# Performance work log

Measured on AMD Instinct MI355X. Metric: run time of the kernel, lower is better.

## Reference

```python
import math
import jax, jax.numpy as jnp
import numpy as np

B, P, DC, NB, H = 32768, 16, 128, 32, 256
BOUND = 10.0
MIN_W = 1e-5
MIN_H = 1e-5
MIN_D = 1e-5
L2PI = 0.5 * math.log(2.0 * math.pi)


def setup_inputs() -> dict:
    key = jax.random.key(0)
    k0, k1, k2, k3 = jax.random.split(key, 4)
    x = jax.random.normal(k0, (B, P, 4), jnp.float32)
    c = jax.random.normal(k1, (B, P, DC), jnp.float32)
    W1 = jax.random.normal(k2, (DC, H), jnp.float32) / np.float32(np.sqrt(DC))
    b1 = jnp.zeros((H,), jnp.float32)
    # small init so spline params start near-identity-ish (typical subnet init)
    W2 = jax.random.normal(k3, (H, 3 * NB + 1), jnp.float32) * np.float32(0.1 / np.sqrt(H))
    b2 = jnp.zeros((3 * NB + 1,), jnp.float32)
    return {"x": x, "c": c, "W1": W1, "b1": b1, "W2": W2, "b2": b2}


def _pad_left_zero(a):
    # pad a zero at the start of the last axis
    pads = [(0, 0)] * (a.ndim - 1) + [(1, 0)]
    return jnp.pad(a, pads)


def _rqs_forward(x, theta):
    """Unconstrained rational-quadratic spline, forward direction.
    x: (B, P); theta: (B, P, 3*NB+1). Returns (z, log|det|), each (B, P)."""
    left, right, bottom, top = -BOUND, BOUND, -BOUND, BOUND
    inside = (x >= left) & (x <= right)

    uw = theta[..., :NB]
    uh = theta[..., NB:2 * NB]
    ud = theta[..., 2 * NB:]  # (B, P, NB+1)

    widths = MIN_W + (1.0 - MIN_W * NB) * jax.nn.softmax(uw, axis=-1)
    cumw = (right - left) * _pad_left_zero(jnp.cumsum(widths, axis=-1)) + left
    cumw = cumw.at[..., 0].set(left).at[..., -1].set(right)
    widths = cumw[..., 1:] - cumw[..., :-1]

    heights = MIN_H + (1.0 - MIN_H * NB) * jax.nn.softmax(uh, axis=-1)
    cumh = (top - bottom) * _pad_left_zero(jnp.cumsum(heights, axis=-1)) + bottom
    cumh = cumh.at[..., 0].set(bottom).at[..., -1].set(top)
    heights = cumh[..., 1:] - cumh[..., :-1]

    derivs = MIN_D + jax.nn.softplus(ud)  # (B, P, NB+1)

    xs = jnp.clip(x, left, right)
    # bin search: index of the bin containing xs
    bin_idx = jnp.clip(jnp.sum(xs[..., None] >= cumw, axis=-1) - 1, 0, NB - 1)
    idx = bin_idx[..., None]

    def g(a):
        return jnp.take_along_axis(a, idx, axis=-1)[..., 0]

    in_cw = g(cumw[..., :-1])
    in_w = g(widths)
    in_ch = g(cumh[..., :-1])
    in_h = g(heights)
    d0 = g(derivs[..., :-1])
    d1 = g(derivs[..., 1:])
    delta = in_h / in_w

    th = (xs - in_cw) / in_w
    th_om = th * (1.0 - th)
    numerator = in_h * (delta * th * th + d0 * th_om)
    denominator = delta + (d0 + d1 - 2.0 * delta) * th_om
    out = in_ch + numerator / denominator

    deriv_num = delta * delta * (d1 * th * th + 2.0 * delta * th_om + d0 * (1.0 - th) ** 2)
    logabsdet = jnp.log(deriv_num) - 2.0 * jnp.log(denominator)

    z = jnp.where(inside, out, x)
    jac = jnp.where(inside, logabsdet, jnp.zeros_like(x))
    return z, jac


def reference(x, c, W1, b1, W2, b2):
    # subnet MLP: c (B, P, DC) -> theta (B, P, 3*NB+1)
    h = jax.nn.relu(jnp.einsum("bpd,dh->bph", c, W1) + b1)
    theta = jnp.einsum("bph,hk->bpk", h, W2) + b2
    z, jac = _rqs_forward(x[..., -1], theta)
    prob = -L2PI - 0.5 * z * z + jac  # (B, P)
    return prob.sum(axis=1)  # (B,)
```

## Files before the change

### kernel.cpp

```cpp
#include <hip/hip_runtime.h>
#include <math.h>

#define NBLK 256
#define NTHR 512
#define PAIRS 8

typedef float  f32x4  __attribute__((ext_vector_type(4)));
typedef float  f32x16 __attribute__((ext_vector_type(16)));
typedef __bf16 bf16x8 __attribute__((ext_vector_type(8)));
typedef unsigned int u32x4 __attribute__((ext_vector_type(4)));

#define W1S 272
#define W2S 528
#define LDS_W1T 0
#define LDS_W2T 69632
#define LDS_B1  137216
#define LDS_B2  138240
#define LDS_TOTAL 138752

#define L2PIF 0.9189385332046727f
#define AW (1.0f - 32.0f*1e-5f)

__device__ __forceinline__ void mfma_v(f32x16& acc, bf16x8 a, bf16x8 b) {
    asm("s_nop 1\n\tv_mfma_f32_32x32x16_bf16 %0, %1, %2, %0"
        : "+v"(acc) : "v"(a), "v"(b));
}
__device__ __forceinline__ void mfma_a(f32x16& acc, bf16x8 a, bf16x8 b) {
    asm("s_nop 1\n\tv_mfma_f32_32x32x16_bf16 %0, %1, %2, %0"
        : "+a"(acc) : "v"(a), "v"(b));
}
__device__ __forceinline__ void mfma_a_init(f32x16& acc, bf16x8 a, bf16x8 b) {
    asm("s_nop 1\n\tv_mfma_f32_32x32x16_bf16 %0, %1, %2, 0"
        : "=a"(acc) : "v"(a), "v"(b));
}
__device__ __forceinline__ void mfma_fence_va(f32x16& v0, f32x16& a1) {
    asm("s_nop 7\n\ts_nop 7\n\ts_nop 7" : "+v"(v0), "+a"(a1));
}
__device__ __forceinline__ void mfma_fence4(f32x16& a0, f32x16& a1,
                                            f32x16& a2, f32x16& a3) {
    asm("s_nop 7\n\ts_nop 7\n\ts_nop 7"
        : "+a"(a0), "+a"(a1), "+a"(a2), "+a"(a3));
}

__device__ __forceinline__ void pl32swap(unsigned &a, unsigned &b) {
#if __has_builtin(__builtin_amdgcn_permlane32_swap)
    auto r = __builtin_amdgcn_permlane32_swap(a, b, false, false);
    a = (unsigned)r[0]; b = (unsigned)r[1];
#else
    asm("v_permlane32_swap_b32 %0, %1" : "+v"(a), "+v"(b));
#endif
}
__device__ __forceinline__ float sum32(float x) {
    unsigned a = __float_as_uint(x), b = a;
    pl32swap(a, b);
    return __uint_as_float(a) + __uint_as_float(b);
}
__device__ __forceinline__ float part32(float x) {
    unsigned u = __float_as_uint(x), a = u, b = u;
    pl32swap(a, b);
    return __uint_as_float(a ^ b ^ u);
}

__device__ __forceinline__ float rcpf(float x) {
#if __has_builtin(__builtin_amdgcn_rcpf)
    return __builtin_amdgcn_rcpf(x);
#else
    return 1.f / x;
#endif
}

template<int CTRL>
__device__ __forceinline__ float dppf(float v) {
    return __int_as_float(__builtin_amdgcn_update_dpp(
        0, __float_as_int(v), CTRL, 0xF, 0xF, false));
}
__device__ __forceinline__ float rorsum16(float x) {
    x += dppf<0x121>(x);
    x += dppf<0x122>(x);
    x += dppf<0x124>(x);
    x += dppf<0x128>(x);
    return x;
}
__device__ __forceinline__ float softplus_s(float u) {
    return fmaxf(u, 0.f) + __logf(1.f + __expf(-fabsf(u)));
}
__device__ __forceinline__ unsigned packbf(float a, float b) {
    unsigned short ua = __builtin_bit_cast(unsigned short, (__bf16)a);
    unsigned short ub = __builtin_bit_cast(unsigned short, (__bf16)b);
    return (unsigned)ua | ((unsigned)ub << 16);
}
__device__ __forceinline__ bf16x8 cvt8(f32x4 a, f32x4 b) {
    bf16x8 r;
    r[0]=(__bf16)a[0]; r[1]=(__bf16)a[1]; r[2]=(__bf16)a[2]; r[3]=(__bf16)a[3];
    r[4]=(__bf16)b[0]; r[5]=(__bf16)b[1]; r[6]=(__bf16)b[2]; r[7]=(__bf16)b[3];
    return r;
}

__device__ __forceinline__ void cum_softmax(const f32x16& tv, const char* bias,
                                            int h, float hf, float hoff,
                                            float* a, float* pw0)
{
    float bs0, bs1, bs2, bs3;
    #pragma unroll
    for (int m = 0; m < 4; ++m) {
        f32x4 bv = *(const f32x4*)(bias + m*32);
        float e0 = __expf(tv[4*m+0] + bv[0]);
        float e1 = __expf(tv[4*m+1] + bv[1]);
        float e2 = __expf(tv[4*m+2] + bv[2]);
        float e3 = __expf(tv[4*m+3] + bv[3]);
        a[4*m+0] = e0; a[4*m+1] = e1; a[4*m+2] = e2; a[4*m+3] = e3;
        float s = (e0 + e1) + (e2 + e3);
        if (m == 0) bs0 = s; else if (m == 1) bs1 = s;
        else if (m == 2) bs2 = s; else bs3 = s;
    }
    float t0 = sum32(bs0), t1 = sum32(bs1), t2 = sum32(bs2), t3 = sum32(bs3);
    float T1 = t0, T2 = T1 + t1, T3 = T2 + t2, S = T3 + t3;
    float sc = (20.f * AW) * rcpf(S);
    float st0 = hf * (t0 - bs0);
    float st1 = T1 + hf * (t1 - bs1);
    float st2 = T2 + hf * (t2 - bs2);
    float st3 = T3 + hf * (t3 - bs3);
    pw0[0] = fmaf(sc, st0, hoff);
    pw0[1] = fmaf(sc, st1, hoff + 1.6e-3f);
    pw0[2] = fmaf(sc, st2, hoff + 3.2e-3f);
    pw0[3] = fmaf(sc, st3, hoff + 4.8e-3f);
    #pragma unroll
    for (int m = 0; m < 4; ++m) {
        float run = (m == 0) ? st0 : (m == 1) ? st1 : (m == 2) ? st2 : st3;
        #pragma unroll
        for (int e = 0; e < 4; ++e) {
            run += a[4*m+e];
            a[4*m+e] = hoff + fmaf(sc, run, 2.0e-4f*(float)(8*m + e + 1));
        }
    }
    if (h) a[15] = 10.f;
}

__global__ __launch_bounds__(NTHR)
__attribute__((amdgpu_waves_per_eu(2)))
void flow_kernel(const float* __restrict__ x, const float* __restrict__ c,
                 const float* __restrict__ W1, const float* __restrict__ b1,
                 const float* __restrict__ W2, const float* __restrict__ b2,
                 float* __restrict__ out)
{
    extern __shared__ char smem[];
    const int tid  = threadIdx.x;
    const int wave = tid >> 6;
    const int lane = tid & 63;
    const int p    = lane & 31;
    const int h    = lane >> 5;
    const float hf   = (float)h;
    const float hoff = h ? (8.0e-4f - 10.f) : -10.f;

    {
        const f32x4* W1v = (const f32x4*)W1;
        for (int it = 0; it < 16; ++it) {
            int f4i = tid + it*NTHR;
            int d  = f4i >> 6;
            int j0 = (f4i & 63) << 2;
            f32x4 v = W1v[f4i];
            #pragma unroll
            for (int e = 0; e < 4; ++e) {
                int j = j0 + e;
                *(__bf16*)(smem + LDS_W1T + j*W1S + d*2) = (__bf16)v[e];
            }
        }
        const f32x4* W2v = (const f32x4*)W2;
        for (int f4i = tid; f4i < 6208; f4i += NTHR) {
            f32x4 v = W2v[f4i];
            #pragma unroll
            for (int e = 0; e < 4; ++e) {
                int lin = f4i*4 + e;
                int j = lin / 97;
                int q = lin - j*97;
                *(__bf16*)(smem + LDS_W2T + q*W2S + j*2) = (__bf16)v[e];
            }
        }
        for (int i = tid; i < 31*256; i += NTHR) {
            int q = 97 + (i >> 8);
            int j = i & 255;
            *(__bf16*)(smem + LDS_W2T + q*W2S + j*2) = (__bf16)0.f;
        }
        float* b1s = (float*)(smem + LDS_B1);
        float* b2s = (float*)(smem + LDS_B2);
        if (tid < 256) b1s[tid] = b1[tid];
        if (tid < 128) b2s[tid] = (tid < 97) ? b2[tid] : 0.f;
    }
    __syncthreads();

    const char* w1b = smem + LDS_W1T + p*W1S + h*16;
    const char* w2b = smem + LDS_W2T + p*W2S + h*16;
    const char* bb1 = smem + LDS_B1 + h*16;
    const char* bb2 = smem + LDS_B2 + h*16;

    const int base = blockIdx.x*128 + wave*16;

    bf16x8 cfrag[8];
    {
        const float* crow = c + (size_t)(base*16 + p)*128 + h*8;
        #pragma unroll
        for (int s = 0; s < 8; ++s)
            cfrag[s] = cvt8(*(const f32x4*)(crow + s*16),
                            *(const f32x4*)(crow + s*16 + 4));
    }
    float xr = x[(size_t)(base*16 + p)*4 + 3];

    for (int itn = 0; itn < PAIRS; ++itn) {
        const int t0 = base + itn*2;
        const int tn = (itn + 1 < PAIRS) ? (t0 + 2) : t0;
        const float* crow_n = c + (size_t)(tn*16 + p)*128 + h*8;

        f32x16 g2[4];
        f32x4  pf[6];
        bf16x8 cfrag_n[8];

        __builtin_amdgcn_s_setprio(1);

        #pragma unroll
        for (int jt = 0; jt < 8; ++jt) {
            pf[(jt % 3)*2]     = *(const f32x4*)(crow_n + jt*16);
            pf[(jt % 3)*2 + 1] = *(const f32x4*)(crow_n + jt*16 + 4);

            f32x16 g1a;
            #pragma unroll
            for (int m = 0; m < 4; ++m) {
                f32x4 bv = *(const f32x4*)(bb1 + jt*128 + m*32);
                g1a[4*m+0] = bv[0]; g1a[4*m+1] = bv[1];
                g1a[4*m+2] = bv[2]; g1a[4*m+3] = bv[3];
            }
            f32x16 g1b;
            #pragma unroll
            for (int s = 0; s < 4; ++s) {
                bf16x8 wa0 = *(const bf16x8*)(w1b + jt*32*W1S + s*32);
                bf16x8 wa1 = *(const bf16x8*)(w1b + jt*32*W1S + (s+4)*32);
                mfma_v(g1a, wa0, cfrag[s]);
                if (s == 0) mfma_a_init(g1b, wa1, cfrag[4]);
                else        mfma_a(g1b, wa1, cfrag[s+4]);
            }
            mfma_fence_va(g1a, g1b);
            unsigned P[8];
            #pragma unroll
            for (int m = 0; m < 4; ++m) {
                float v0 = fmaxf(g1a[4*m+0] + g1b[4*m+0], 0.f);
                float v1 = fmaxf(g1a[4*m+1] + g1b[4*m+1], 0.f);
                float v2 = fmaxf(g1a[4*m+2] + g1b[4*m+2], 0.f);
                float v3 = fmaxf(g1a[4*m+3] + g1b[4*m+3], 0.f);
                P[2*m]   = packbf(v0, v1);
                P[2*m+1] = packbf(v2, v3);
            }
            #pragma unroll
            for (int cc = 0; cc < 2; ++cc) {
                unsigned fa = P[4*cc+0], fb = P[4*cc+2];
                pl32swap(fa, fb);
                unsigned fc = P[4*cc+1], fd = P[4*cc+3];
                pl32swap(fc, fd);
                u32x4 fr;
                fr[0] = fa; fr[1] = fc; fr[2] = fb; fr[3] = fd;
                bf16x8 hb = __builtin_bit_cast(bf16x8, fr);
                const int kc = 2*jt + cc;
                #pragma unroll
                for (int qt = 0; qt < 4; ++qt) {
                    bf16x8 wb = *(const bf16x8*)(w2b + qt*32*W2S + kc*32);
                    if (jt == 0 && cc == 0) mfma_a_init(g2[qt], wb, hb);
                    else                    mfma_a(g2[qt], wb, hb);
                }
            }
            if (jt >= 2) {
                const int s = jt - 2;
                cfrag_n[s] = cvt8(pf[(s % 3)*2], pf[(s % 3)*2 + 1]);
            }
        }
        __builtin_amdgcn_s_setprio(0);

        cfrag_n[6] = cvt8(pf[(6 % 3)*2], pf[(6 % 3)*2 + 1]);
        cfrag_n[7] = cvt8(pf[(7 % 3)*2], pf[(7 % 3)*2 + 1]);

        mfma_fence4(g2[0], g2[1], g2[2], g2[3]);

        const float xr_cur = xr;
        float xn = x[(size_t)(tn*16 + p)*4 + 3];

        const float xs = fminf(fmaxf(xr_cur, -10.f), 10.f);
        unsigned selm = 0;
        float a_cw = 0.f, a_cwp = 0.f;
        {
            float cw[16], pw0[4];
            cum_softmax(g2[0], bb2, h, hf, hoff, cw, pw0);
            #pragma unroll
            for (int r = 0; r < 16; ++r) {
                const int m = r >> 2;
                float pw = (r & 3) ? cw[r-1] : pw0[m];
                bool sel = (xs >= pw) && ((xs < cw[r]) || (h && r == 15));
                float mf = sel ? 1.f : 0.f;
                a_cw  = fmaf(mf, pw,    a_cw);
                a_cwp = fmaf(mf, cw[r], a_cwp);
                selm |= (sel ? 1u : 0u) << r;
            }
            a_cw  = sum32(a_cw);
            a_cwp = sum32(a_cwp);
        }
        float a_ch = 0.f, a_chp = 0.f;
        {
            float ch[16], ph0[4];
            cum_softmax(g2[1], bb2 + 128, h, hf, hoff, ch, ph0);
            #pragma unroll
            for (int r = 0; r < 16; ++r) {
                const int m = r >> 2;
                float ph = (r & 3) ? ch[r-1] : ph0[m];
                float mf = (float)((selm >> r) & 1u);
                a_ch  = fmaf(mf, ph,    a_ch);
                a_chp = fmaf(mf, ch[r], a_chp);
            }
            a_ch  = sum32(a_ch);
            a_chp = sum32(a_chp);
        }
        float a_d0 = 0.f, a_d1 = 0.f;
        {
            float dv[16];
            #pragma unroll
            for (int m = 0; m < 4; ++m) {
                f32x4 bv = *(const f32x4*)(bb2 + 256 + m*32);
                #pragma unroll
                for (int e = 0; e < 4; ++e)
                    dv[4*m+e] = 1e-5f + softplus_s(g2[2][4*m+e] + bv[e]);
            }
            float d32 = 1e-5f + softplus_s(g2[3][0]
                                           + *(const float*)(smem + LDS_B2 + 384));
            float Z[4];
            #pragma unroll
            for (int m = 0; m < 4; ++m) Z[m] = part32(dv[4*m]);
            float Z4 = part32(d32);
            #pragma unroll
            for (int r = 0; r < 16; ++r) {
                const int m = r >> 2;
                float nd = ((r & 3) < 3) ? dv[r+1] : (h ? ((m < 3) ? Z[m+1] : Z4) : Z[m]);
                float mf = (float)((selm >> r) & 1u);
                a_d0 = fmaf(mf, dv[r], a_d0);
                a_d1 = fmaf(mf, nd,    a_d1);
            }
            a_d0 = sum32(a_d0);
            a_d1 = sum32(a_d1);
        }

        float val;
        if (xr_cur >= -10.f && xr_cur <= 10.f) {
            float in_w  = a_cwp - a_cw;
            float in_h  = a_chp - a_ch;
            float rw    = rcpf(in_w);
            float delta = in_h * rw;
            float tt    = (xs - a_cw) * rw;
            float thom  = tt * (1.f - tt);
            float den   = delta + (a_d0 + a_d1 - 2.f*delta)*thom;
            float rden  = rcpf(den);
            float z     = fmaf(in_h*(delta*tt*tt + a_d0*thom), rden, a_ch);
            float omt   = 1.f - tt;
            float dnum  = delta*delta*(a_d1*tt*tt + 2.f*delta*thom + a_d0*omt*omt);
            val = -L2PIF - 0.5f*z*z + __logf(dnum) - 2.f*__logf(den);
        } else {
            val = -L2PIF - 0.5f*xr_cur*xr_cur;
        }

        val = rorsum16(val);
        if (lane == 0)  out[t0]     = val;
        if (lane == 16) out[t0 + 1] = val;

        xr = xn;
        #pragma unroll
        for (int s = 0; s < 8; ++s) cfrag[s] = cfrag_n[s];
    }
}

extern "C" void kernel_launch(void* const* d_in, const int* in_sizes, int n_in,
                              void* d_out, int out_size, void* d_ws, size_t ws_size,
                              hipStream_t stream) {
    (void)in_sizes; (void)n_in; (void)out_size; (void)d_ws; (void)ws_size;
    const float* x  = (const float*)d_in[0];
    const float* c  = (const float*)d_in[1];
    const float* W1 = (const float*)d_in[2];
    const float* b1 = (const float*)d_in[3];
    const float* W2 = (const float*)d_in[4];
    const float* b2 = (const float*)d_in[5];
    float* out = (float*)d_out;

    (void)hipFuncSetAttribute((const void*)flow_kernel,
                              hipFuncAttributeMaxDynamicSharedMemorySize, LDS_TOTAL);

    flow_kernel<<<NBLK, NTHR, LDS_TOTAL, stream>>>(x, c, W1, b1, W2, b2, out);
}
```

Baseline: 99.88 us.

## Software-pipeline second GEMM one step behind first, drop MFMA nops, tree-reduce selects

```diff
diff --git a/kernel.cpp b/kernel.cpp
--- a/kernel.cpp
+++ b/kernel.cpp
@@ -25,12 +25,20 @@
     asm("s_nop 1\n\tv_mfma_f32_32x32x16_bf16 %0, %1, %2, %0"
         : "+v"(acc) : "v"(a), "v"(b));
 }
-__device__ __forceinline__ void mfma_a(f32x16& acc, bf16x8 a, bf16x8 b) {
+__device__ __forceinline__ void mfma_v_f(f32x16& acc, bf16x8 a, bf16x8 b) {
+    asm("v_mfma_f32_32x32x16_bf16 %0, %1, %2, %0"
+        : "+v"(acc) : "v"(a), "v"(b));
+}
+__device__ __forceinline__ void mfma_a_f(f32x16& acc, bf16x8 a, bf16x8 b) {
+    asm("v_mfma_f32_32x32x16_bf16 %0, %1, %2, %0"
+        : "+a"(acc) : "v"(a), "v"(b));
+}
+__device__ __forceinline__ void mfma_a_n(f32x16& acc, bf16x8 a, bf16x8 b) {
     asm("s_nop 1\n\tv_mfma_f32_32x32x16_bf16 %0, %1, %2, %0"
         : "+a"(acc) : "v"(a), "v"(b));
 }
 __device__ __forceinline__ void mfma_a_init(f32x16& acc, bf16x8 a, bf16x8 b) {
-    asm("s_nop 1\n\tv_mfma_f32_32x32x16_bf16 %0, %1, %2, 0"
+    asm("v_mfma_f32_32x32x16_bf16 %0, %1, %2, 0"
         : "=a"(acc) : "v"(a), "v"(b));
 }
 __device__ __forceinline__ void mfma_fence_va(f32x16& v0, f32x16& a1) {
@@ -94,6 +102,11 @@
     r[0]=(__bf16)a[0]; r[1]=(__bf16)a[1]; r[2]=(__bf16)a[2]; r[3]=(__bf16)a[3];
     r[4]=(__bf16)b[0]; r[5]=(__bf16)b[1]; r[6]=(__bf16)b[2]; r[7]=(__bf16)b[3];
     return r;
+}
+__device__ __forceinline__ float tree16(const float* t) {
+    float a0 = t[0]+t[1],  a1 = t[2]+t[3],  a2 = t[4]+t[5],  a3 = t[6]+t[7];
+    float b0 = t[8]+t[9],  b1 = t[10]+t[11], b2 = t[12]+t[13], b3 = t[14]+t[15];
+    return ((a0+a1)+(a2+a3)) + ((b0+b1)+(b2+b3));
 }
 
 __device__ __forceinline__ void cum_softmax(const f32x16& tv, const char* bias,
@@ -192,6 +205,7 @@
     const char* w2b = smem + LDS_W2T + p*W2S + h*16;
     const char* bb1 = smem + LDS_B1 + h*16;
     const char* bb2 = smem + LDS_B2 + h*16;
+    const float b96v = *(const float*)(smem + LDS_B2 + 384);
 
     const int base = blockIdx.x*128 + wave*16;
 
@@ -213,6 +227,7 @@
         f32x16 g2[4];
         f32x4  pf[6];
         bf16x8 cfrag_n[8];
+        u32x4  hbp[2];
 
         __builtin_amdgcn_s_setprio(1);
 
@@ -233,9 +248,23 @@
             for (int s = 0; s < 4; ++s) {
                 bf16x8 wa0 = *(const bf16x8*)(w1b + jt*32*W1S + s*32);
                 bf16x8 wa1 = *(const bf16x8*)(w1b + jt*32*W1S + (s+4)*32);
-                mfma_v(g1a, wa0, cfrag[s]);
-                if (s == 0) mfma_a_init(g1b, wa1, cfrag[4]);
-                else        mfma_a(g1b, wa1, cfrag[s+4]);
+                if (s == 0) { mfma_v(g1a, wa0, cfrag[0]);
+                              mfma_a_init(g1b, wa1, cfrag[4]); }
+                else        { mfma_v_f(g1a, wa0, cfrag[s]);
+                              mfma_a_f(g1b, wa1, cfrag[s+4]); }
+            }
+            if (jt >= 1) {
+                #pragma unroll
+                for (int cc = 0; cc < 2; ++cc) {
+                    bf16x8 hb = __builtin_bit_cast(bf16x8, hbp[cc]);
+                    const int kc = 2*(jt-1) + cc;
+                    #pragma unroll
+                    for (int qt = 0; qt < 4; ++qt) {
+                        bf16x8 wb = *(const bf16x8*)(w2b + qt*32*W2S + kc*32);
+                        if (jt == 1 && cc == 0) mfma_a_init(g2[qt], wb, hb);
+                        else                    mfma_a_f(g2[qt], wb, hb);
+                    }
+                }
             }
             mfma_fence_va(g1a, g1b);
             unsigned P[8];
@@ -256,35 +285,41 @@
                 pl32swap(fc, fd);
                 u32x4 fr;
                 fr[0] = fa; fr[1] = fc; fr[2] = fb; fr[3] = fd;
-                bf16x8 hb = __builtin_bit_cast(bf16x8, fr);
-                const int kc = 2*jt + cc;
-                #pragma unroll
-                for (int qt = 0; qt < 4; ++qt) {
-                    bf16x8 wb = *(const bf16x8*)(w2b + qt*32*W2S + kc*32);
-                    if (jt == 0 && cc == 0) mfma_a_init(g2[qt], wb, hb);
-                    else                    mfma_a(g2[qt], wb, hb);
-                }
+                hbp[cc] = fr;
             }
             if (jt >= 2) {
                 const int s = jt - 2;
                 cfrag_n[s] = cvt8(pf[(s % 3)*2], pf[(s % 3)*2 + 1]);
             }
         }
+        #pragma unroll
+        for (int cc = 0; cc < 2; ++cc) {
+            bf16x8 hb = __builtin_bit_cast(bf16x8, hbp[cc]);
+            const int kc = 14 + cc;
+            #pragma unroll
+            for (int qt = 0; qt < 4; ++qt) {
+                bf16x8 wb = *(const bf16x8*)(w2b + qt*32*W2S + kc*32);
+                if (qt == 0) mfma_a_n(g2[qt], wb, hb);
+                else         mfma_a_f(g2[qt], wb, hb);
+            }
+        }
         __builtin_amdgcn_s_setprio(0);
 
-        cfrag_n[6] = cvt8(pf[(6 % 3)*2], pf[(6 % 3)*2 + 1]);
-        cfrag_n[7] = cvt8(pf[(7 % 3)*2], pf[(7 % 3)*2 + 1]);
-
-        mfma_fence4(g2[0], g2[1], g2[2], g2[3]);
+        if (itn + 1 < PAIRS) {
+            cfrag_n[6] = cvt8(pf[(6 % 3)*2], pf[(6 % 3)*2 + 1]);
+            cfrag_n[7] = cvt8(pf[(7 % 3)*2], pf[(7 % 3)*2 + 1]);
+        }
 
         const float xr_cur = xr;
         float xn = x[(size_t)(tn*16 + p)*4 + 3];
 
+        mfma_fence4(g2[0], g2[1], g2[2], g2[3]);
+
         const float xs = fminf(fmaxf(xr_cur, -10.f), 10.f);
         unsigned selm = 0;
-        float a_cw = 0.f, a_cwp = 0.f;
+        float a_cw, a_cwp;
         {
-            float cw[16], pw0[4];
+            float cw[16], pw0[4], tw[16], twp[16];
             cum_softmax(g2[0], bb2, h, hf, hoff, cw, pw0);
             #pragma unroll
             for (int r = 0; r < 16; ++r) {
@@ -292,31 +327,31 @@
                 float pw = (r & 3) ? cw[r-1] : pw0[m];
                 bool sel = (xs >= pw) && ((xs < cw[r]) || (h && r == 15));
                 float mf = sel ? 1.f : 0.f;
-                a_cw  = fmaf(mf, pw,    a_cw);
-                a_cwp = fmaf(mf, cw[r], a_cwp);
+                tw[r]  = mf * pw;
+                twp[r] = mf * cw[r];
                 selm |= (sel ? 1u : 0u) << r;
             }
-            a_cw  = sum32(a_cw);
-            a_cwp = sum32(a_cwp);
-        }
-        float a_ch = 0.f, a_chp = 0.f;
+            a_cw  = sum32(tree16(tw));
+            a_cwp = sum32(tree16(twp));
+        }
+        float a_ch, a_chp;
         {
-            float ch[16], ph0[4];
+            float ch[16], ph0[4], th[16], thp[16];
             cum_softmax(g2[1], bb2 + 128, h, hf, hoff, ch, ph0);
             #pragma unroll
             for (int r = 0; r < 16; ++r) {
                 const int m = r >> 2;
                 float ph = (r & 3) ? ch[r-1] : ph0[m];
                 float mf = (float)((selm >> r) & 1u);
-                a_ch  = fmaf(mf, ph,    a_ch);
-                a_chp = fmaf(mf, ch[r], a_chp);
-            }
-            a_ch  = sum32(a_ch);
-            a_chp = sum32(a_chp);
-        }
-        float a_d0 = 0.f, a_d1 = 0.f;
+                th[r]  = mf * ph;
+                thp[r] = mf * ch[r];
+            }
+            a_ch  = sum32(tree16(th));
+            a_chp = sum32(tree16(thp));
+        }
+        float a_d0, a_d1;
         {
-            float dv[16];
+            float dv[16], td0[16], td1[16];
             #pragma unroll
             for (int m = 0; m < 4; ++m) {
                 f32x4 bv = *(const f32x4*)(bb2 + 256 + m*32);
@@ -324,8 +359,7 @@
                 for (int e = 0; e < 4; ++e)
                     dv[4*m+e] = 1e-5f + softplus_s(g2[2][4*m+e] + bv[e]);
             }
-            float d32 = 1e-5f + softplus_s(g2[3][0]
-                                           + *(const float*)(smem + LDS_B2 + 384));
+            float d32 = 1e-5f + softplus_s(g2[3][0] + b96v);
             float Z[4];
             #pragma unroll
             for (int m = 0; m < 4; ++m) Z[m] = part32(dv[4*m]);
@@ -335,11 +369,11 @@
                 const int m = r >> 2;
                 float nd = ((r & 3) < 3) ? dv[r+1] : (h ? ((m < 3) ? Z[m+1] : Z4) : Z[m]);
                 float mf = (float)((selm >> r) & 1u);
-                a_d0 = fmaf(mf, dv[r], a_d0);
-                a_d1 = fmaf(mf, nd,    a_d1);
-            }
-            a_d0 = sum32(a_d0);
-            a_d1 = sum32(a_d1);
+                td0[r] = mf * dv[r];
+                td1[r] = mf * nd;
+            }
+            a_d0 = sum32(tree16(td0));
+            a_d1 = sum32(tree16(td1));
         }
 
         float val;
@@ -365,8 +399,10 @@
         if (lane == 16) out[t0 + 1] = val;
 
         xr = xn;
-        #pragma unroll
-        for (int s = 0; s < 8; ++s) cfrag[s] = cfrag_n[s];
+        if (itn + 1 < PAIRS) {
+            #pragma unroll
+            for (int s = 0; s < 8; ++s) cfrag[s] = cfrag_n[s];
+        }
     }
 }
 
```

Result: slower. 116.2 us (+16.4%).
